# Performance work log

Hardware: AMD Instinct MI355X
Metric: run time of the kernel (lower is better)

The kernel has to match this reference:

```python
import jax, jax.numpy as jnp
import numpy as np

EPS = 1e-5
K_PATCHES = 5000  # sample_pixels // 16


def _resize_bilinear(x, h, w):
    # matches torch F.interpolate(mode='bilinear', align_corners=False)
    return jax.image.resize(x, (x.shape[0], x.shape[1], h, w), method="bilinear", antialias=False)


def _bn(x, g, b, m, v):
    # eval-mode BatchNorm2d with running stats
    inv = jax.lax.rsqrt(v + EPS)
    return (x - m[None, :, None, None]) * (g * inv)[None, :, None, None] + b[None, :, None, None]


def _conv(x, w):
    return jax.lax.conv_general_dilated(x, w, (1, 1), "VALID",
                                        dimension_numbers=("NCHW", "OIHW", "NCHW"))


def setup_inputs():
    key = jax.random.key(0)
    ks = jax.random.split(key, 14)
    B, Hc, Wc = 2, 512, 512
    pha = jax.random.uniform(ks[0], (B, 1, Hc, Wc), jnp.float32)
    err = jax.random.uniform(ks[1], (B, 1, Hc, Wc), jnp.float32)  # strictly >0 so mask is all-ones
    hid = jax.random.normal(ks[2], (B, 32, Hc, Wc), jnp.float32)

    def conv_w(k, o, i):
        return jax.random.normal(k, (o, i, 3, 3), jnp.float32) * 0.05

    def bn_p(k, c):
        k1, k2 = jax.random.split(k)
        return (1.0 + 0.1 * jax.random.normal(k1, (c,), jnp.float32),
                0.1 * jax.random.normal(k2, (c,), jnp.float32),
                jnp.zeros((c,), jnp.float32), jnp.ones((c,), jnp.float32))

    g1, b1, m1, v1 = bn_p(ks[4], 24)
    g2, b2, m2, v2 = bn_p(ks[6], 16)
    g3, b3, m3, v3 = bn_p(ks[8], 12)
    return dict(pha=pha, err=err, hid=hid,
                w1=conv_w(ks[3], 24, 33), g1=g1, b1=b1, m1=m1, v1=v1,
                w2=conv_w(ks[5], 16, 24), g2=g2, b2=b2, m2=m2, v2=v2,
                w3=conv_w(ks[7], 12, 16), g3=g3, b3=b3, m3=m3, v3=v3,
                w4=conv_w(ks[9], 1, 12),
                b4=0.1 * jax.random.normal(ks[10], (1,), jnp.float32),
                H_full=2048, W_full=2048)


def reference(pha, err, hid, w1, g1, b1, m1, v1, w2, g2, b2, m2, v2,
              w3, g3, b3, m3, v3, w4, b4, H_full, W_full):
    B = pha.shape[0]
    Hh, Wh = H_full // 2, W_full // 2
    Hq, Wq = H_full // 4, W_full // 4

    # --- select_refinement_regions (sampling mode) ---
    err_q = _resize_bilinear(err, Hq, Wq)                      # (B,1,Hq,Wq)
    flat = err_q.reshape(B, -1)
    _, top_idx = jax.lax.top_k(flat, K_PATCHES)                # (B,K)
    ref = jnp.zeros_like(flat).at[jnp.arange(B)[:, None], top_idx].set(1.0)
    ref = ref * (flat > 0).astype(flat.dtype)                  # prevent_oversampling
    ref = ref.reshape(B, 1, Hq, Wq)

    # nonzero(ref) == topk locations here (err is strictly positive)
    bidx = jnp.repeat(jnp.arange(B), K_PATCHES)                # (P,)
    hidx = (top_idx // Wq).reshape(-1)                         # (P,)
    widx = (top_idx % Wq).reshape(-1)                          # (P,)

    # --- crop_patch (unfold-equivalent gather), size=2, padding=3 ---
    x = jnp.concatenate([hid, pha], axis=1)                    # (B,33,Hc,Wc)
    x = _resize_bilinear(x, Hh, Wh)                            # (B,33,Hh,Wh)
    pad, size = 3, 2
    win = size + 2 * pad                                       # 8
    xp = jnp.pad(x, ((0, 0), (0, 0), (pad, pad), (pad, pad)))
    rows = hidx[:, None] * size + jnp.arange(win)              # (P,8)
    cols = widx[:, None] * size + jnp.arange(win)              # (P,8)
    patches = xp[bidx[:, None, None], :, rows[:, :, None], cols[:, None, :]]  # (P,8,8,33)
    patches = patches.transpose(0, 3, 1, 2)                    # (P,33,8,8)

    # --- small conv stack ---
    y = jax.nn.relu(_bn(_conv(patches, w1), g1, b1, m1, v1))   # (P,24,6,6)
    y = jax.nn.relu(_bn(_conv(y, w2), g2, b2, m2, v2))         # (P,16,4,4)
    y = jnp.repeat(jnp.repeat(y, 2, axis=2), 2, axis=3)        # nearest -> (P,16,8,8)
    y = jax.nn.relu(_bn(_conv(y, w3), g3, b3, m3, v3))         # (P,12,6,6)
    y = _conv(y, w4) + b4[None, :, None, None]                 # (P,1,4,4)

    # --- replace_patch (scatter_nd of 4x4 blocks into full-res pha) ---
    pha_full = _resize_bilinear(pha, H_full, W_full)           # (B,1,H,W)
    pr = hidx[:, None, None] * 4 + jnp.arange(4)[None, :, None]  # (P,4,1)
    pc = widx[:, None, None] * 4 + jnp.arange(4)[None, None, :]  # (P,1,4)
    pha_full = pha_full.at[bidx[:, None, None], 0, pr, pc].set(y[:, 0])
    return pha_full, ref
```

## Files before the change

kernel.cpp:

```cpp
#include <hip/hip_runtime.h>
#include <stdint.h>

#define K_SEL 5000
#define NQ    262144
#define NB    2

#define BIAS_OFF 38912
#define W4_OFF   39424
#define ST_OFF   40960

#define WS_HIST 16
#define WS_SEL  2064
#define WS_EQ   12064
#define EQ_CAP  4096

typedef _Float16 f16x8 __attribute__((ext_vector_type(8)));
typedef _Float16 f16x4 __attribute__((ext_vector_type(4)));
typedef float    f32x4 __attribute__((ext_vector_type(4)));
#define MFMA16(a,b,c) __builtin_amdgcn_mfma_f32_16x16x32_f16(a,b,c,0,0,0)

__global__ void prep_kernel(const float* __restrict__ w1, const float* __restrict__ g1,
                            const float* __restrict__ b1, const float* __restrict__ m1,
                            const float* __restrict__ v1,
                            const float* __restrict__ w2, const float* __restrict__ g2,
                            const float* __restrict__ b2, const float* __restrict__ m2,
                            const float* __restrict__ v2,
                            const float* __restrict__ w3, const float* __restrict__ g3,
                            const float* __restrict__ b3, const float* __restrict__ m3,
                            const float* __restrict__ v3,
                            const float* __restrict__ w4, const float* __restrict__ b4,
                            char* __restrict__ ws) {
    _Float16* wf = (_Float16*)ws;
    float* bias = (float*)(ws + BIAS_OFF);
    float* w4r  = (float*)(ws + W4_OFF);
    uint32_t* st = (uint32_t*)(ws + ST_OFF);
    int tid = threadIdx.x;
    for (int t = tid; t < 38 * 512; t += 256) {
        int frag = t >> 9, li = (t >> 3) & 63, j = t & 7;
        int lo = li & 15, hi = li >> 4;
        float val = 0.f;
        if (frag < 18) {
            int ky = frag / 6, r = frag % 6, kx = r >> 1, mt = r & 1;
            int oc = mt * 16 + lo, ci = hi * 8 + j;
            if (oc < 24) val = w1[((oc * 33 + ci) * 3 + ky) * 3 + kx] * g1[oc] * rsqrtf(v1[oc] + 1e-5f);
        } else if (frag < 27) {
            int f = frag - 18, ky = f / 3, kt = f % 3;
            int oc = lo, k = kt * 32 + hi * 8 + j;
            if (k < 72) {
                int kx = k / 24, ci = k % 24;
                val = w2[((oc * 24 + ci) * 3 + ky) * 3 + kx] * g2[oc] * rsqrtf(v2[oc] + 1e-5f);
            }
        } else if (frag < 36) {
            int s = frag - 27, ky = s / 3, kx = s % 3;
            int oc = lo, ci = hi * 8 + j;
            if (oc < 12 && ci < 16) val = w3[((oc * 16 + ci) * 3 + ky) * 3 + kx] * g3[oc] * rsqrtf(v3[oc] + 1e-5f);
        } else {
            int mt = frag - 36, oc = mt * 16 + lo, tap = hi * 8 + j;
            if (oc < 24 && tap < 9)
                val = w1[((oc * 33 + 32) * 3 + tap / 3) * 3 + tap % 3] * g1[oc] * rsqrtf(v1[oc] + 1e-5f);
        }
        wf[t] = (_Float16)val;
    }
    if (tid < 53) {
        float v;
        if (tid < 24)      { float sc = g1[tid] * rsqrtf(v1[tid] + 1e-5f); v = b1[tid] - m1[tid] * sc; }
        else if (tid < 40) { int c = tid - 24; float sc = g2[c] * rsqrtf(v2[c] + 1e-5f); v = b2[c] - m2[c] * sc; }
        else if (tid < 52) { int c = tid - 40; float sc = g3[c] * rsqrtf(v3[c] + 1e-5f); v = b3[c] - m3[c] * sc; }
        else v = b4[0];
        bias[tid] = v;
    }
    if (tid < 144) { int t9 = tid / 16, ci = tid % 16; w4r[tid] = (ci < 12) ? w4[ci * 9 + t9] : 0.f; }
    for (int i = tid; i < WS_HIST + 4 * 512; i += 256) st[i] = 0u;
    __syncthreads();
    if (tid == 0) { st[2] = K_SEL; st[3] = K_SEL; }
}

__global__ void hist_kernel(const float* __restrict__ err, uint32_t* st, int round) {
    __shared__ uint32_t h[256];
    h[threadIdx.x] = 0u;
    __syncthreads();
    int t = blockIdx.x * 256 + threadIdx.x;
    int b = t >> 18;
    uint32_t bits = __float_as_uint(err[t]);
    uint32_t pref = st[b];
    int shift = 24 - 8 * round;
    bool match = (round == 0) || ((bits >> (shift + 8)) == (pref >> (shift + 8)));
    if (match) atomicAdd(&h[(bits >> shift) & 255u], 1u);
    __syncthreads();
    uint32_t v = h[threadIdx.x];
    if (v) atomicAdd(&st[WS_HIST + round * 512 + b * 256 + threadIdx.x], v);
}

__global__ void scan_kernel(uint32_t* st, int round) {
    int b = blockIdx.x;
    int lane = threadIdx.x;
    int shift = 24 - 8 * round;
    const uint32_t* hist = st + WS_HIST + round * 512 + b * 256;
    int binbase = 255 - 4 * lane;
    uint32_t hv0 = hist[binbase], hv1 = hist[binbase - 1],
             hv2 = hist[binbase - 2], hv3 = hist[binbase - 3];
    uint32_t p = hv0 + hv1 + hv2 + hv3;
    uint32_t cum = p;
    for (int o = 1; o < 64; o <<= 1) {
        uint32_t n = __shfl_up(cum, o);
        if (lane >= o) cum += n;
    }
    uint32_t rem = st[2 + b];
    unsigned long long bal = __ballot(cum >= rem);
    int first = __ffsll(bal) - 1;
    if (lane == first) {
        uint32_t acc = cum - p;
        uint32_t hv[4] = {hv0, hv1, hv2, hv3};
        int chosen = binbase;
        for (int q = 0; q < 4; q++) {
            if (acc + hv[q] >= rem) { chosen = binbase - q; break; }
            acc += hv[q];
        }
        uint32_t pref = st[b] | ((uint32_t)chosen << shift);
        st[b] = pref;
        st[2 + b] = rem - acc;
        if (round == 3) { st[4 + b] = pref; st[6 + b] = rem - acc; }
    }
}

__global__ void compact_kernel(const float* __restrict__ err, uint32_t* st,
                               float* __restrict__ refout) {
    __shared__ uint32_t selbuf[512];
    __shared__ uint32_t eqbuf[512];
    __shared__ uint32_t cnts[2];
    __shared__ uint32_t bases[2];
    int blk = blockIdx.x;
    int b = blk >> 9;
    int base = (blk & 511) << 9;
    if (threadIdx.x < 2) cnts[threadIdx.x] = 0u;
    __syncthreads();
    uint32_t T = st[4 + b];
#pragma unroll
    for (int it = 0; it < 2; it++) {
        int i = base + it * 256 + threadIdx.x;
        uint32_t bits = __float_as_uint(err[b * NQ + i]);
        float rv = 0.f;
        if (bits > T) {
            rv = 1.0f;
            uint32_t s = atomicAdd(&cnts[0], 1u);
            selbuf[s] = (uint32_t)i;
        } else if (bits == T) {
            uint32_t e = atomicAdd(&cnts[1], 1u);
            eqbuf[e] = (uint32_t)i;
        }
        refout[b * NQ + i] = rv;
    }
    __syncthreads();
    if (threadIdx.x == 0 && cnts[0]) bases[0] = atomicAdd(&st[8 + b], cnts[0]);
    if (threadIdx.x == 1 && cnts[1]) bases[1] = atomicAdd(&st[10 + b], cnts[1]);
    __syncthreads();
    for (uint32_t j = threadIdx.x; j < cnts[0]; j += 256) {
        uint32_t slot = bases[0] + j;
        if (slot < K_SEL) st[WS_SEL + b * K_SEL + slot] = selbuf[j];
    }
    for (uint32_t j = threadIdx.x; j < cnts[1]; j += 256) {
        uint32_t slot = bases[1] + j;
        if (slot < EQ_CAP) st[WS_EQ + b * EQ_CAP + slot] = eqbuf[j];
    }
}

__global__ void select_kernel(uint32_t* st, float* __restrict__ refout) {
    __shared__ uint32_t L[EQ_CAP];
    int b = blockIdx.x;
    uint32_t m = st[10 + b]; if (m > EQ_CAP) m = EQ_CAP;
    uint32_t need = st[6 + b];
    uint32_t T = st[4 + b];
    for (uint32_t j = threadIdx.x; j < m; j += blockDim.x) L[j] = st[WS_EQ + b * EQ_CAP + j];
    __syncthreads();
    for (uint32_t j = threadIdx.x; j < m; j += blockDim.x) {
        uint32_t idx = L[j];
        uint32_t rank = 0;
        for (uint32_t q = 0; q < m; q++) rank += (L[q] < idx) ? 1u : 0u;
        if (rank < need) {
            uint32_t slot = atomicAdd(&st[8 + b], 1u);
            if (slot < K_SEL) st[WS_SEL + b * K_SEL + slot] = idx;
            refout[b * NQ + idx] = (T != 0u) ? 1.0f : 0.0f;
        }
    }
}

__global__ void upsample_kernel(const float* __restrict__ pha, float* __restrict__ out) {
    int t = blockIdx.x * 256 + threadIdx.x;
    int xq = t & 511;
    int rest = t >> 9;
    int oy = rest & 2047;
    int b  = rest >> 11;
    const float* src = pha + (size_t)b * NQ;
    float sy = oy * 0.25f - 0.375f;
    sy = fminf(fmaxf(sy, 0.0f), 511.0f);
    int y0 = (int)sy; int y1i = min(y0 + 1, 511);
    float fy = sy - (float)y0;
    float rv[4];
#pragma unroll
    for (int j = 0; j < 4; j++) {
        int ox = xq * 4 + j;
        float sx = ox * 0.25f - 0.375f;
        sx = fminf(fmaxf(sx, 0.0f), 511.0f);
        int x0 = (int)sx; int x1i = min(x0 + 1, 511);
        float fx = sx - (float)x0;
        float v00 = src[y0 * 512 + x0],  v01 = src[y0 * 512 + x1i];
        float v10 = src[y1i * 512 + x0], v11 = src[y1i * 512 + x1i];
        rv[j] = v00 * (1.f - fy) * (1.f - fx) + v01 * (1.f - fy) * fx
              + v10 * fy * (1.f - fx)         + v11 * fy * fx;
    }
    float4 r4 = make_float4(rv[0], rv[1], rv[2], rv[3]);
    *reinterpret_cast<float4*>(out + (size_t)b * 4194304 + (size_t)oy * 2048 + xq * 4) = r4;
}

__device__ __forceinline__ f16x8 ldfrag(const _Float16* wf, int frag, int l) {
    return *(const f16x8*)(wf + frag * 512 + l * 8);
}

__global__ __launch_bounds__(128) void patch_kernel(
    const float* __restrict__ hid, const float* __restrict__ pha,
    const char* __restrict__ ws, float* __restrict__ out) {
    __shared__ _Float16 xs[64][40];
    __shared__ _Float16 y1n[36][40];
    __shared__ _Float16 pool[64][40];
    __shared__ float pha8[64];
    __shared__ float biasL[56];
    float* y3s = (float*)&y1n[0][0];

    const _Float16* wf = (const _Float16*)ws;
    const float* biasG = (const float*)(ws + BIAS_OFF);
    const float* w4r   = (const float*)(ws + W4_OFF);
    const uint32_t* st = (const uint32_t*)(ws + ST_OFF);

    int tid = threadIdx.x, l = tid & 63, wid = tid >> 6;
    int lo = l & 15, hi = l >> 4;
    int bp = blockIdx.x;
    int b = (bp >= K_SEL) ? 1 : 0;
    int pi = bp - b * K_SEL;
    uint32_t idx = st[WS_SEL + b * K_SEL + pi] & 0x3FFFFu;
    int hq = (int)(idx >> 9), wq = (int)(idx & 511u);

    if (tid < 53) biasL[tid] = biasG[tid];

    int ry = l >> 3, rx = l & 7;
    int hy = hq * 2 + ry - 3, hx = wq * 2 + rx - 3;
    bool inb = ((unsigned)hy < 1024u) && ((unsigned)hx < 1024u);
    float sy = fminf(fmaxf(hy * 0.5f - 0.25f, 0.f), 511.f);
    float sx = fminf(fmaxf(hx * 0.5f - 0.25f, 0.f), 511.f);
    int y0 = (int)sy, x0 = (int)sx;
    int y1c = min(y0 + 1, 511), x1c = min(x0 + 1, 511);
    float fy = sy - (float)y0, fx = sx - (float)x0;
    int o00 = y0 * 512 + x0, o01 = y0 * 512 + x1c, o10 = y1c * 512 + x0, o11 = y1c * 512 + x1c;
    float w00 = (1.f - fy) * (1.f - fx), w01 = (1.f - fy) * fx;
    float w10 = fy * (1.f - fx), w11 = fy * fx;

    _Float16 hv[16];
    {
        const float* hb = hid + ((size_t)b * 32 + wid * 16) * NQ;
#pragma unroll
        for (int c = 0; c < 16; c++) {
            const float* p = hb + (size_t)c * NQ;
            float v = 0.f;
            if (inb) v = p[o00] * w00 + p[o01] * w01 + p[o10] * w10 + p[o11] * w11;
            hv[c] = (_Float16)v;
        }
    }
    f16x8 h0 = {hv[0], hv[1], hv[2], hv[3], hv[4], hv[5], hv[6], hv[7]};
    f16x8 h1 = {hv[8], hv[9], hv[10], hv[11], hv[12], hv[13], hv[14], hv[15]};
    {
        _Float16* xrow = &xs[l][wid * 16];
        *(f16x8*)xrow = h0;
        *((f16x8*)xrow + 1) = h1;
    }
    f16x8 z8 = {(_Float16)0.f, (_Float16)0.f, (_Float16)0.f, (_Float16)0.f,
                (_Float16)0.f, (_Float16)0.f, (_Float16)0.f, (_Float16)0.f};
    if (wid == 1) {
        const float* p = pha + (size_t)b * NQ;
        float v = 0.f;
        if (inb) v = p[o00] * w00 + p[o01] * w01 + p[o10] * w10 + p[o11] * w11;
        pha8[l] = v;
    }
    __syncthreads();

    if (wid == 0) {
        if (l < 48) {
            int py = (l * 43) >> 8, px = l - py * 6;
            _Float16 tap[9];
#pragma unroll
            for (int t = 0; t < 9; t++) {
                int ky = t / 3, kx = t % 3;
                int ip = (py + ky) * 8 + px + kx;
                tap[t] = (_Float16)pha8[ip & 63];
            }
            _Float16* row = &pool[l][0];
            f16x8 r0 = {tap[0], tap[1], tap[2], tap[3], tap[4], tap[5], tap[6], tap[7]};
            f16x8 r1 = z8; r1[0] = tap[8];
            *(f16x8*)row = r0;
            *(f16x8*)(row + 8)  = r1;
            *(f16x8*)(row + 16) = z8;
            *(f16x8*)(row + 24) = z8;
        }
    } else {
        for (int i = l; i < 72; i += 64) {
            *(f16x8*)&y1n[i >> 1][24 + (i & 1) * 8] = z8;
        }
    }
    __syncthreads();

    f32x4 zf = {0.f, 0.f, 0.f, 0.f};
    f32x4 aA0 = zf, aA1 = zf, aB = zf;
    int nA = wid * 16 + lo, nB = 32 + lo;
    int pyA = (nA * 43) >> 8, pxA = nA - pyA * 6;
    int pyB = (nB * 43) >> 8, pxB = nB - pyB * 6;
    {
        f16x8 A0 = ldfrag(wf, 36, l), A1 = ldfrag(wf, 37, l);
        f16x8 BA = *(const f16x8*)&pool[nA][hi * 8];
        f16x8 BB = *(const f16x8*)&pool[nB][hi * 8];
        aA0 = MFMA16(A0, BA, aA0);
        aA1 = MFMA16(A1, BA, aA1);
        aB  = MFMA16(wid ? A1 : A0, BB, aB);
    }
#pragma unroll
    for (int ky = 0; ky < 3; ky++) {
#pragma unroll
        for (int kt = 0; kt < 3; kt++) {
            f16x8 A0 = ldfrag(wf, ky * 6 + kt * 2 + 0, l);
            f16x8 A1 = ldfrag(wf, ky * 6 + kt * 2 + 1, l);
            int rA = ((pyA + ky) * 8 + pxA + kt) & 63;
            int rB = ((pyB + ky) * 8 + pxB + kt) & 63;
            f16x8 BA = *(const f16x8*)&xs[rA][hi * 8];
            f16x8 BB = *(const f16x8*)&xs[rB][hi * 8];
            aA0 = MFMA16(A0, BA, aA0);
            aA1 = MFMA16(A1, BA, aA1);
            aB  = MFMA16(wid ? A1 : A0, BB, aB);
        }
    }
    {
        f32x4 accs[3] = {aA0, aA1, aB};
        int mts[3] = {0, 1, wid};
        int nts[3] = {wid, wid, 2};
#pragma unroll
        for (int f = 0; f < 3; f++) {
            int n = nts[f] * 16 + lo;
            int ocb = mts[f] * 16 + hi * 4;
            if (n < 36 && ocb < 24) {
                f16x4 hh;
                hh[0] = (_Float16)fmaxf(accs[f][0] + biasL[ocb + 0], 0.f);
                hh[1] = (_Float16)fmaxf(accs[f][1] + biasL[ocb + 1], 0.f);
                hh[2] = (_Float16)fmaxf(accs[f][2] + biasL[ocb + 2], 0.f);
                hh[3] = (_Float16)fmaxf(accs[f][3] + biasL[ocb + 3], 0.f);
                *(f16x4*)&y1n[n][ocb] = hh;
            }
        }
    }
    __syncthreads();

    if (wid == 0) {
        f32x4 a2 = zf;
        int qy = lo >> 2, qx = lo & 3;
#pragma unroll
        for (int ky = 0; ky < 3; ky++) {
#pragma unroll
            for (int kt = 0; kt < 3; kt++) {
                f16x8 A = ldfrag(wf, 18 + ky * 3 + kt, l);
                int k = kt * 32 + hi * 8;
                const _Float16* bptr;
                if (k < 72) {
                    int kx = k / 24, ci0 = k - kx * 24;
                    bptr = &y1n[(qy + ky) * 6 + qx + kx][ci0];
                } else {
                    bptr = &y1n[0][24];
                }
                f16x8 B = *(const f16x8*)bptr;
                a2 = MFMA16(A, B, a2);
            }
        }
        int ocb = hi * 4;
        f16x4 hh;
        hh[0] = (_Float16)fmaxf(a2[0] + biasL[24 + ocb + 0], 0.f);
        hh[1] = (_Float16)fmaxf(a2[1] + biasL[24 + ocb + 1], 0.f);
        hh[2] = (_Float16)fmaxf(a2[2] + biasL[24 + ocb + 2], 0.f);
        hh[3] = (_Float16)fmaxf(a2[3] + biasL[24 + ocb + 3], 0.f);
#pragma unroll
        for (int dy = 0; dy < 2; dy++)
#pragma unroll
            for (int dx = 0; dx < 2; dx++) {
                int row = (2 * qy + dy) * 8 + 2 * qx + dx;
                *(f16x4*)&pool[row][ocb] = hh;
            }
    } else {
        *(f16x8*)&pool[l][16] = z8;
        *(f16x8*)&pool[l][24] = z8;
    }
    __syncthreads();

    f32x4 aC = zf, aD = zf;
    int nC = wid * 16 + lo, nD = 32 + lo;
    int pyC = (nC * 43) >> 8, pxC = nC - pyC * 6;
    int pyD = (nD * 43) >> 8, pxD = nD - pyD * 6;
#pragma unroll
    for (int s = 0; s < 9; s++) {
        int ky = s / 3, kx = s % 3;
        f16x8 A = ldfrag(wf, 27 + s, l);
        f16x8 BC = *(const f16x8*)&pool[((pyC + ky) * 8 + pxC + kx) & 63][hi * 8];
        aC = MFMA16(A, BC, aC);
        if (wid) {
            f16x8 BD = *(const f16x8*)&pool[((pyD + ky) * 8 + pxD + kx) & 63][hi * 8];
            aD = MFMA16(A, BD, aD);
        }
    }
    __syncthreads();
    {
        int ocb = hi * 4;
        f32x4 accs[2] = {aC, aD};
        int nts[2] = {wid, 2};
        int cnt = wid ? 2 : 1;
        for (int f = 0; f < cnt; f++) {
            int n = nts[f] * 16 + lo;
            if (n < 36) {
                f32x4 v;
#pragma unroll
                for (int r = 0; r < 4; r++) {
                    float bb = (ocb + r < 12) ? biasL[40 + ocb + r] : 0.f;
                    float x = accs[f][r] + bb;
                    v[r] = (ocb + r < 12) ? fmaxf(x, 0.f) : 0.f;
                }
                *(f32x4*)&y3s[n * 16 + ocb] = v;
            }
        }
    }
    __syncthreads();

    if (wid == 0) {
        int r4 = lo >> 2, c4 = lo & 3, cig = hi;
        float acc = 0.f;
#pragma unroll
        for (int t = 0; t < 9; t++) {
            int ky = t / 3, kx = t % 3;
            const f32x4 xv = *(const f32x4*)&y3s[((r4 + ky) * 6 + c4 + kx) * 16 + cig * 4];
            const f32x4 wv = *(const f32x4*)(w4r + t * 16 + cig * 4);
            acc += xv[0] * wv[0] + xv[1] * wv[1] + xv[2] * wv[2] + xv[3] * wv[3];
        }
        acc += __shfl_xor(acc, 32);
        acc += __shfl_xor(acc, 16);
        if (l < 16) {
            out[(size_t)b * 4194304 + (size_t)(hq * 4 + r4) * 2048 + (wq * 4 + c4)] = acc + biasL[52];
        }
    }
}

extern "C" void kernel_launch(void* const* d_in, const int* in_sizes, int n_in,
                              void* d_out, int out_size, void* d_ws, size_t ws_size,
                              hipStream_t stream) {
    const float* pha = (const float*)d_in[0];
    const float* err = (const float*)d_in[1];
    const float* hid = (const float*)d_in[2];
    const float* w1  = (const float*)d_in[3];
    const float* g1  = (const float*)d_in[4];
    const float* bb1 = (const float*)d_in[5];
    const float* m1  = (const float*)d_in[6];
    const float* v1  = (const float*)d_in[7];
    const float* w2  = (const float*)d_in[8];
    const float* g2  = (const float*)d_in[9];
    const float* bb2 = (const float*)d_in[10];
    const float* m2  = (const float*)d_in[11];
    const float* v2  = (const float*)d_in[12];
    const float* w3  = (const float*)d_in[13];
    const float* g3  = (const float*)d_in[14];
    const float* bb3 = (const float*)d_in[15];
    const float* m3  = (const float*)d_in[16];
    const float* v3  = (const float*)d_in[17];
    const float* w4  = (const float*)d_in[18];
    const float* b4  = (const float*)d_in[19];

    float* out    = (float*)d_out;
    float* refout = out + (size_t)NB * 4194304;
    char* ws      = (char*)d_ws;
    uint32_t* st  = (uint32_t*)(ws + ST_OFF);

    prep_kernel<<<1, 256, 0, stream>>>(w1, g1, bb1, m1, v1, w2, g2, bb2, m2, v2,
                                       w3, g3, bb3, m3, v3, w4, b4, ws);
    for (int r = 0; r < 4; r++) {
        hist_kernel<<<2048, 256, 0, stream>>>(err, st, r);
        scan_kernel<<<2, 64, 0, stream>>>(st, r);
    }
    compact_kernel<<<1024, 256, 0, stream>>>(err, st, refout);
    select_kernel<<<2, 256, 0, stream>>>(st, refout);
    upsample_kernel<<<8192, 256, 0, stream>>>(pha, out);
    patch_kernel<<<2 * K_SEL, 128, 0, stream>>>(hid, pha, ws, out);
}
```

Measured before the change: 166.3 us.

## Replace atomic stream compaction with count, scan and place kernels

The single compaction kernel, which used shared and global atomics to claim output slots, is split into three kernels. The first counts selected elements per block with wavefront ballots, the second prefix-scans the block counts, and the third writes indices to deterministic, index-ordered slots. This removes the global atomic contention on the selection counter and makes the selected patch order follow spatial order, which may help locality in the patch kernel. The cost is two extra kernel launches and a second full read of the error map.

```diff
diff --git a/kernel.cpp b/kernel.cpp
--- a/kernel.cpp
+++ b/kernel.cpp
@@ -9,10 +9,12 @@
 #define W4_OFF   39424
 #define ST_OFF   40960
 
-#define WS_HIST 16
-#define WS_SEL  2064
-#define WS_EQ   12064
-#define EQ_CAP  4096
+#define WS_HIST  16
+#define WS_SEL   2064
+#define WS_EQ    12064
+#define EQ_CAP   4096
+#define WS_BCNT  20480
+#define WS_BBASE 21504
 
 typedef _Float16 f16x8 __attribute__((ext_vector_type(8)));
 typedef _Float16 f16x4 __attribute__((ext_vector_type(4)));
@@ -123,45 +125,74 @@
     }
 }
 
-__global__ void compact_kernel(const float* __restrict__ err, uint32_t* st,
-                               float* __restrict__ refout) {
-    __shared__ uint32_t selbuf[512];
-    __shared__ uint32_t eqbuf[512];
-    __shared__ uint32_t cnts[2];
-    __shared__ uint32_t bases[2];
-    int blk = blockIdx.x;
-    int b = blk >> 9;
-    int base = (blk & 511) << 9;
-    if (threadIdx.x < 2) cnts[threadIdx.x] = 0u;
-    __syncthreads();
+__global__ void ccount_kernel(const float* __restrict__ err, uint32_t* st) {
+    __shared__ uint32_t wsum[8];
+    int blk = blockIdx.x, tid = threadIdx.x;
+    int b = blk >> 9, base = (blk & 511) << 9;
     uint32_t T = st[4 + b];
-#pragma unroll
-    for (int it = 0; it < 2; it++) {
-        int i = base + it * 256 + threadIdx.x;
-        uint32_t bits = __float_as_uint(err[b * NQ + i]);
-        float rv = 0.f;
-        if (bits > T) {
-            rv = 1.0f;
-            uint32_t s = atomicAdd(&cnts[0], 1u);
-            selbuf[s] = (uint32_t)i;
-        } else if (bits == T) {
-            uint32_t e = atomicAdd(&cnts[1], 1u);
-            eqbuf[e] = (uint32_t)i;
-        }
-        refout[b * NQ + i] = rv;
-    }
-    __syncthreads();
-    if (threadIdx.x == 0 && cnts[0]) bases[0] = atomicAdd(&st[8 + b], cnts[0]);
-    if (threadIdx.x == 1 && cnts[1]) bases[1] = atomicAdd(&st[10 + b], cnts[1]);
-    __syncthreads();
-    for (uint32_t j = threadIdx.x; j < cnts[0]; j += 256) {
-        uint32_t slot = bases[0] + j;
-        if (slot < K_SEL) st[WS_SEL + b * K_SEL + slot] = selbuf[j];
-    }
-    for (uint32_t j = threadIdx.x; j < cnts[1]; j += 256) {
-        uint32_t slot = bases[1] + j;
-        if (slot < EQ_CAP) st[WS_EQ + b * EQ_CAP + slot] = eqbuf[j];
-    }
+    uint32_t b0 = __float_as_uint(err[b * NQ + base + tid]);
+    uint32_t b1 = __float_as_uint(err[b * NQ + base + 256 + tid]);
+    unsigned long long m0 = __ballot(b0 > T);
+    unsigned long long m1 = __ballot(b1 > T);
+    int w = tid >> 6, lane = tid & 63;
+    if (lane == 0) { wsum[w] = (uint32_t)__popcll(m0); wsum[4 + w] = (uint32_t)__popcll(m1); }
+    __syncthreads();
+    if (tid == 0)
+        st[WS_BCNT + blk] = wsum[0] + wsum[1] + wsum[2] + wsum[3]
+                          + wsum[4] + wsum[5] + wsum[6] + wsum[7];
+}
+
+__global__ void cscan_kernel(uint32_t* st) {
+    __shared__ uint32_t wtot[8];
+    int b = blockIdx.x, tid = threadIdx.x;
+    int lane = tid & 63, w = tid >> 6;
+    uint32_t v = st[WS_BCNT + b * 512 + tid];
+    uint32_t inc = v;
+    for (int o = 1; o < 64; o <<= 1) {
+        uint32_t n = __shfl_up(inc, o);
+        if (lane >= o) inc += n;
+    }
+    if (lane == 63) wtot[w] = inc;
+    __syncthreads();
+    uint32_t off = 0;
+    for (int j = 0; j < w; j++) off += wtot[j];
+    uint32_t base = off + inc - v;
+    st[WS_BBASE + b * 512 + tid] = base;
+    if (tid == 511) st[8 + b] = base + v;
+}
+
+__global__ void cplace_kernel(const float* __restrict__ err, uint32_t* st,
+                              float* __restrict__ refout) {
+    __shared__ uint32_t wc[8];
+    int blk = blockIdx.x, tid = threadIdx.x;
+    int b = blk >> 9, base = (blk & 511) << 9;
+    uint32_t T = st[4 + b];
+    uint32_t blkbase = st[WS_BBASE + b * 512 + (blk & 511)];
+    int i0 = base + tid, i1 = base + 256 + tid;
+    uint32_t b0 = __float_as_uint(err[b * NQ + i0]);
+    uint32_t b1 = __float_as_uint(err[b * NQ + i1]);
+    bool s0 = b0 > T, s1 = b1 > T;
+    unsigned long long m0 = __ballot(s0);
+    unsigned long long m1 = __ballot(s1);
+    int w = tid >> 6, lane = tid & 63;
+    if (lane == 0) { wc[w] = (uint32_t)__popcll(m0); wc[4 + w] = (uint32_t)__popcll(m1); }
+    refout[b * NQ + i0] = s0 ? 1.0f : 0.0f;
+    refout[b * NQ + i1] = s1 ? 1.0f : 0.0f;
+    __syncthreads();
+    uint32_t tot0 = wc[0] + wc[1] + wc[2] + wc[3];
+    uint32_t pre0 = 0, pre1 = tot0;
+    for (int j = 0; j < w; j++) { pre0 += wc[j]; pre1 += wc[4 + j]; }
+    unsigned long long lt = (1ull << lane) - 1ull;
+    if (s0) {
+        uint32_t slot = blkbase + pre0 + (uint32_t)__popcll(m0 & lt);
+        if (slot < K_SEL) st[WS_SEL + b * K_SEL + slot] = (uint32_t)i0;
+    }
+    if (s1) {
+        uint32_t slot = blkbase + pre1 + (uint32_t)__popcll(m1 & lt);
+        if (slot < K_SEL) st[WS_SEL + b * K_SEL + slot] = (uint32_t)i1;
+    }
+    if (b0 == T) { uint32_t e = atomicAdd(&st[10 + b], 1u); if (e < EQ_CAP) st[WS_EQ + b * EQ_CAP + e] = (uint32_t)i0; }
+    if (b1 == T) { uint32_t e = atomicAdd(&st[10 + b], 1u); if (e < EQ_CAP) st[WS_EQ + b * EQ_CAP + e] = (uint32_t)i1; }
 }
 
 __global__ void select_kernel(uint32_t* st, float* __restrict__ refout) {
@@ -483,7 +514,9 @@
         hist_kernel<<<2048, 256, 0, stream>>>(err, st, r);
         scan_kernel<<<2, 64, 0, stream>>>(st, r);
     }
-    compact_kernel<<<1024, 256, 0, stream>>>(err, st, refout);
+    ccount_kernel<<<1024, 256, 0, stream>>>(err, st);
+    cscan_kernel<<<2, 512, 0, stream>>>(st);
+    cplace_kernel<<<1024, 256, 0, stream>>>(err, st, refout);
     select_kernel<<<2, 256, 0, stream>>>(st, refout);
     upsample_kernel<<<8192, 256, 0, stream>>>(pha, out);
     patch_kernel<<<2 * K_SEL, 128, 0, stream>>>(hid, pha, ws, out);
```

Result: faster. 158.7 us (-4.6%).
